# Kernel optimization log

Measured on AMD Instinct MI355X. Metric: run time of the kernel, lower is better.

## Reference

```python
import jax, jax.numpy as jnp
import numpy as np

B, S, D, H, F = 4, 2048, 512, 8, 2048
HD = D // H
EPS = 1e-5


def setup_inputs() -> dict:
    key = jax.random.key(0)
    ks = jax.random.split(key, 12)
    s = lambda fan_in: 1.0 / np.sqrt(fan_in)
    return {
        "x": jax.random.normal(ks[0], (B, S, D), dtype=jnp.float32),
        "Wqkv": jax.random.uniform(ks[1], (D, 3 * D), minval=-s(D), maxval=s(D)),
        "bqkv": jax.random.uniform(ks[2], (3 * D,), minval=-s(D), maxval=s(D)),
        "Wo": jax.random.uniform(ks[3], (D, D), minval=-s(D), maxval=s(D)),
        "bo": jax.random.uniform(ks[4], (D,), minval=-s(D), maxval=s(D)),
        "g1": jnp.ones((D,), jnp.float32),
        "beta1": jnp.zeros((D,), jnp.float32),
        "W1": jax.random.uniform(ks[5], (D, F), minval=-s(D), maxval=s(D)),
        "b1": jax.random.uniform(ks[6], (F,), minval=-s(D), maxval=s(D)),
        "W2": jax.random.uniform(ks[7], (F, D), minval=-s(F), maxval=s(F)),
        "b2": jax.random.uniform(ks[8], (D,), minval=-s(F), maxval=s(F)),
        "g2": jnp.ones((D,), jnp.float32),
        "beta2": jnp.zeros((D,), jnp.float32),
    }


def _layernorm(x, g, b):
    mu = jnp.mean(x, axis=-1, keepdims=True)
    var = jnp.mean(jnp.square(x - mu), axis=-1, keepdims=True)
    return (x - mu) * jax.lax.rsqrt(var + EPS) * g + b


def reference(x, Wqkv, bqkv, Wo, bo, g1, beta1, W1, b1, W2, b2, g2, beta2):
    b, s, d = x.shape
    # QKV projection -> [b, s, 3, H, HD] -> q,k,v each [b, H, s, HD]
    qkv = (x @ Wqkv + bqkv).reshape(b, s, 3, H, HD)
    q, k, v = jnp.moveaxis(qkv, 2, 0)            # [3, b, s, H, HD]
    q = q.transpose(0, 2, 1, 3)
    k = k.transpose(0, 2, 1, 3)
    v = v.transpose(0, 2, 1, 3)
    scores = jnp.einsum('bhqd,bhkd->bhqk', q, k) / np.sqrt(HD).astype(np.float32)
    attn = jax.nn.softmax(scores, axis=-1)
    ctx = jnp.einsum('bhqk,bhkd->bhqd', attn, v)
    ctx = ctx.transpose(0, 2, 1, 3).reshape(b, s, d)
    attn_out = ctx @ Wo + bo
    x = _layernorm(x + attn_out, g1, beta1)
    # FFN (dropout inactive in eval)
    ffn = jax.nn.relu(x @ W1 + b1) @ W2 + b2
    return _layernorm(x + ffn, g2, beta2)
```

## Files before the change

### kernel.cpp

```cpp
#include <hip/hip_runtime.h>
#include <hip/hip_bf16.h>

#define S_ 2048
#define M_ 8192

typedef __bf16 bf16x8 __attribute__((ext_vector_type(8)));
typedef float f32x4 __attribute__((ext_vector_type(4)));

__device__ __forceinline__ void gload16(const void* g, void* l) {
  __builtin_amdgcn_global_load_lds(
      (const __attribute__((address_space(1))) void*)g,
      (__attribute__((address_space(3))) void*)l, 16, 0, 0);
}

template<int CTRL>
__device__ __forceinline__ float dppf(float x) {
  return __int_as_float(__builtin_amdgcn_update_dpp(
      0, __float_as_int(x), CTRL, 0xF, 0xF, true));
}
__device__ __forceinline__ float red16_sum(float x) {
  x += dppf<0x121>(x);
  x += dppf<0x122>(x);
  x += dppf<0x124>(x);
  x += dppf<0x128>(x);
  return x;
}

__global__ __launch_bounds__(256)
void cvt_x_k(const float* __restrict__ x, __bf16* __restrict__ xb) {
  int i = blockIdx.x * 256 + threadIdx.x;
  float4 v = ((const float4*)x)[i];
  union { __bf16 hh[4]; uint2 u; } pk;
  pk.hh[0] = (__bf16)v.x; pk.hh[1] = (__bf16)v.y;
  pk.hh[2] = (__bf16)v.z; pk.hh[3] = (__bf16)v.w;
  ((uint2*)xb)[i] = pk.u;
}

__global__ __launch_bounds__(256)
void tcvt_k(const float* __restrict__ Wm, __bf16* __restrict__ Wt, int K, int N) {
  __shared__ float tile[64][65];
  int nbn = N >> 6;
  int tk = blockIdx.x / nbn, tn = blockIdx.x % nbn;
  int tc = threadIdx.x & 63, tr = threadIdx.x >> 6;
#pragma unroll
  for (int p = 0; p < 16; ++p) {
    int kl = p * 4 + tr;
    tile[kl][tc] = Wm[(size_t)(tk * 64 + kl) * N + tn * 64 + tc];
  }
  __syncthreads();
#pragma unroll
  for (int p = 0; p < 16; ++p) {
    int nl = p * 4 + tr;
    Wt[(size_t)(tn * 64 + nl) * K + tk * 64 + tc] = (__bf16)tile[tc][nl];
  }
}

template<int MODE, int N, int K, int BM, int KS = 1>
__global__ __launch_bounds__(256, 2)
void gemm_k(const __bf16* __restrict__ A, const __bf16* __restrict__ Bt,
            const float* __restrict__ bias,
            float* __restrict__ outf, __bf16* __restrict__ outb,
            __bf16* __restrict__ outq, __bf16* __restrict__ outk,
            __bf16* __restrict__ outv) {
  constexpr int NB = N / 128;
  constexpr int BJ = (BM == 128) ? 4 : 2;
  constexpr int KT = K / KS / 64;
  __shared__ __bf16 As[BM * 64];
  __shared__ __bf16 Bs[128 * 64];

  int id = blockIdx.x;
  int cpx = gridDim.x >> 3;
  int sw = (id & 7) * cpx + (id >> 3);
  int ks = 0;
  if (KS == 2) { ks = sw & 1; sw >>= 1; }
  int mb = sw / NB, nb = sw % NB;

  int t = threadIdx.x;
  int lane = t & 63;
  int g = lane >> 4, c = lane & 15;
  int w = t >> 6;
  int wrow = (BM == 128) ? (w >> 1) * 64 : 0;
  int wcol = (BM == 128) ? (w & 1) * 64 : w * 32;

  const __bf16* Ab = A + (size_t)mb * BM * K + (size_t)ks * (K / KS);
  const __bf16* Bb = Bt + (size_t)nb * 128 * K + (size_t)ks * (K / KS);

  f32x4 acc[4][BJ] = {};

  for (int kt = 0; kt < KT; ++kt) {
#pragma unroll
    for (int it = 0; it < BM / 32; ++it) {
      int idx = it * 256 + t;
      int row = idx >> 3, ch = idx & 7;
      int sch = ch ^ (row & 7);
      gload16(Ab + (size_t)row * K + kt * 64 + sch * 8, (char*)As + idx * 16);
    }
#pragma unroll
    for (int it = 0; it < 4; ++it) {
      int idx = it * 256 + t;
      int row = idx >> 3, ch = idx & 7;
      int sch = ch ^ (row & 7);
      gload16(Bb + (size_t)row * K + kt * 64 + sch * 8, (char*)Bs + idx * 16);
    }
    __syncthreads();
#pragma unroll
    for (int kk = 0; kk < 2; ++kk) {
      bf16x8 af[4], bfv[BJ];
#pragma unroll
      for (int i = 0; i < 4; ++i) {
        int row = wrow + i * 16 + c;
        int ch = (kk * 4 + g) ^ (row & 7);
        af[i] = *(const bf16x8*)((const char*)As + row * 128 + ch * 16);
      }
#pragma unroll
      for (int j = 0; j < BJ; ++j) {
        int row = wcol + j * 16 + c;
        int ch = (kk * 4 + g) ^ (row & 7);
        bfv[j] = *(const bf16x8*)((const char*)Bs + row * 128 + ch * 16);
      }
      __builtin_amdgcn_s_setprio(1);
#pragma unroll
      for (int i = 0; i < 4; ++i)
#pragma unroll
        for (int j = 0; j < BJ; ++j)
          acc[i][j] = __builtin_amdgcn_mfma_f32_16x16x32_bf16(af[i], bfv[j],
                                                              acc[i][j], 0, 0, 0);
      __builtin_amdgcn_s_setprio(0);
    }
    __syncthreads();
  }

  int row0 = mb * BM + wrow;
  int col0 = nb * 128 + wcol;

  if (MODE == 1) {
#pragma unroll
    for (int j = 0; j < BJ; ++j) {
      int col = col0 + j * 16 + c;
      float bv = bias[col];
#pragma unroll
      for (int i = 0; i < 4; ++i)
#pragma unroll
        for (int r = 0; r < 4; ++r) {
          int rr = row0 + i * 16 + g * 4 + r;
          outf[(size_t)rr * N + col] = acc[i][j][r] + bv;
        }
    }
  } else if (MODE == 2 || MODE == 3) {
    __bf16* dst = (KS == 2 && ks == 1) ? outq : outb;
#pragma unroll
    for (int j = 0; j < BJ; ++j) {
      int col = col0 + j * 16 + c;
      float bv = (KS == 2 && ks == 1) ? 0.f : bias[col];
#pragma unroll
      for (int i = 0; i < 4; ++i)
#pragma unroll
        for (int r = 0; r < 4; ++r) {
          int rr = row0 + i * 16 + g * 4 + r;
          float v = acc[i][j][r] + bv;
          if (MODE == 2) v = fmaxf(v, 0.f);
          dst[(size_t)rr * N + col] = (__bf16)v;
        }
    }
  } else {
    int tsel = nb >> 2;
    int h = ((nb & 3) << 1) | (w & 1);
#pragma unroll
    for (int j = 0; j < BJ; ++j) {
      int hd = j * 16 + c;
      float bv = bias[nb * 128 + wcol + j * 16 + c];
#pragma unroll
      for (int i = 0; i < 4; ++i) {
        int rr = row0 + i * 16 + g * 4;
        int b = rr >> 11, s = rr & 2047;
        int bh = b * 8 + h;
        if (tsel == 2) {
          union { __bf16 hh[4]; uint2 u; } pk;
#pragma unroll
          for (int r = 0; r < 4; ++r) pk.hh[r] = (__bf16)(acc[i][j][r] + bv);
          *(uint2*)(outv + ((size_t)bh * 64 + hd) * 2048 + s) = pk.u;
        } else {
          __bf16* dst = (tsel == 0 ? outq : outk);
#pragma unroll
          for (int r = 0; r < 4; ++r)
            dst[((size_t)bh * 2048 + s + r) * 64 + hd] = (__bf16)(acc[i][j][r] + bv);
        }
      }
    }
  }
}

__global__ __launch_bounds__(256, 4)
void attn_k(const __bf16* __restrict__ qb, const __bf16* __restrict__ kb,
            const __bf16* __restrict__ vt, __bf16* __restrict__ ctx) {
  __shared__ __bf16 Ks[2][64 * 64];
  __shared__ __bf16 Vs[2][64 * 64];
  __shared__ char P_lds[4][16 * 128];

  int id = blockIdx.x;
  int sw = (id & 7) * 128 + (id >> 3);
  int bh = sw >> 5, qblk = sw & 31;

  int t = threadIdx.x, lane = t & 63, w = t >> 6;
  int g = lane >> 4, c = lane & 15;

  const __bf16* Q  = qb + (size_t)bh * S_ * 64;
  const __bf16* Kp = kb + (size_t)bh * S_ * 64;
  const __bf16* Vp = vt + (size_t)bh * 64 * S_;

  int q0 = qblk * 64 + w * 16;

  bf16x8 qf[2];
#pragma unroll
  for (int kk = 0; kk < 2; ++kk) {
    bf16x8 v = *(const bf16x8*)(Q + (size_t)(q0 + c) * 64 + kk * 32 + g * 8);
#pragma unroll
    for (int e = 0; e < 8; ++e) v[e] = (__bf16)((float)v[e] * 0.18033688f);
    qf[kk] = v;
  }

  f32x4 o[4] = {};
  float srun[4] = {0.f, 0.f, 0.f, 0.f};

  char* Pw = P_lds[w];
  int kvoff[2];
#pragma unroll
  for (int kk = 0; kk < 2; ++kk)
    kvoff[kk] = c * 128 + ((kk * 4 + g) ^ (c & 7)) * 16;

  auto stage = [&](int kt, int buf) {
    int kbase = kt * 64;
#pragma unroll
    for (int it = 0; it < 2; ++it) {
      int idx = it * 256 + t;
      int row = idx >> 3, ch = idx & 7;
      int sch = ch ^ (row & 7);
      gload16(Kp + (size_t)(kbase + row) * 64 + sch * 8, (char*)Ks[buf] + idx * 16);
      gload16(Vp + (size_t)row * S_ + kbase + sch * 8,   (char*)Vs[buf] + idx * 16);
    }
  };

  stage(0, 0);

  auto step = [&](int kbi, int cur, bool last) {
    if (!last) stage(kbi + 1, cur ^ 1);
    if (last) asm volatile("s_waitcnt vmcnt(0)" ::: "memory");
    else      asm volatile("s_waitcnt vmcnt(4)" ::: "memory");
    __builtin_amdgcn_s_barrier();
    asm volatile("" ::: "memory");
    const char* Kb = (const char*)Ks[cur];
    const char* Vb = (const char*)Vs[cur];

    bf16x8 kf[4][2];
#pragma unroll
    for (int j = 0; j < 4; ++j)
#pragma unroll
      for (int kk = 0; kk < 2; ++kk)
        kf[j][kk] = *(const bf16x8*)(Kb + j * 2048 + kvoff[kk]);
    f32x4 sacc[4] = {};
    __builtin_amdgcn_s_setprio(1);
#pragma unroll
    for (int j = 0; j < 4; ++j) {
      sacc[j] = __builtin_amdgcn_mfma_f32_16x16x32_bf16(qf[0], kf[j][0], sacc[j], 0, 0, 0);
      sacc[j] = __builtin_amdgcn_mfma_f32_16x16x32_bf16(qf[1], kf[j][1], sacc[j], 0, 0, 0);
    }
    __builtin_amdgcn_s_setprio(0);

#pragma unroll
    for (int r = 0; r < 4; ++r) {
      float p0 = exp2f(sacc[0][r]);
      float p1 = exp2f(sacc[1][r]);
      float p2 = exp2f(sacc[2][r]);
      float p3 = exp2f(sacc[3][r]);
      srun[r] += (p0 + p1) + (p2 + p3);
      int prow = g * 4 + r;
      char* base = Pw + prow * 128;
      int sz = (prow & 7) << 4;
      *(__bf16*)(base + ((2 * c) ^ sz))      = (__bf16)p0;
      *(__bf16*)(base + ((32 + 2 * c) ^ sz)) = (__bf16)p1;
      *(__bf16*)(base + ((64 + 2 * c) ^ sz)) = (__bf16)p2;
      *(__bf16*)(base + ((96 + 2 * c) ^ sz)) = (__bf16)p3;
    }
#pragma unroll
    for (int kk = 0; kk < 2; ++kk) {
      int pch = (kk * 4 + g) ^ (c & 7);
      bf16x8 pf = *(const bf16x8*)(Pw + c * 128 + pch * 16);
      __builtin_amdgcn_s_setprio(1);
#pragma unroll
      for (int n = 0; n < 4; ++n) {
        bf16x8 vf = *(const bf16x8*)(Vb + n * 2048 + kvoff[kk]);
        o[n] = __builtin_amdgcn_mfma_f32_16x16x32_bf16(pf, vf, o[n], 0, 0, 0);
      }
      __builtin_amdgcn_s_setprio(0);
    }
    if (!last) {
      asm volatile("" ::: "memory");
      __builtin_amdgcn_s_barrier();
      asm volatile("" ::: "memory");
    }
  };

  for (int kbi = 0; kbi < 30; kbi += 2) {
    step(kbi, 0, false);
    step(kbi + 1, 1, false);
  }
  step(30, 0, false);
  step(31, 1, true);

  int b = bh >> 3, h = bh & 7;
  f32x4 inv;
#pragma unroll
  for (int r = 0; r < 4; ++r) inv[r] = 1.f / red16_sum(srun[r]);
#pragma unroll
  for (int n = 0; n < 4; ++n)
#pragma unroll
    for (int r = 0; r < 4; ++r) {
      int q = q0 + g * 4 + r;
      int d = n * 16 + c;
      ctx[((size_t)(b * 2048 + q)) * 512 + h * 64 + d] = (__bf16)(o[n][r] * inv[r]);
    }
}

template<bool IN1F32, bool WF, bool IN3>
__global__ __launch_bounds__(256)
void ln_k(const float* __restrict__ in1f, const __bf16* __restrict__ in1b,
          const __bf16* __restrict__ in2, const __bf16* __restrict__ in3,
          const float* __restrict__ gam, const float* __restrict__ bet,
          float* __restrict__ outf, __bf16* __restrict__ outb) {
  int w = threadIdx.x >> 6, lane = threadIdx.x & 63;
  int row = blockIdx.x * 4 + w;
  size_t base = (size_t)row * 512 + lane * 8;
  float a[8];
  if (IN1F32) {
    float4 a0 = *(const float4*)(in1f + base);
    float4 a1 = *(const float4*)(in1f + base + 4);
    a[0] = a0.x; a[1] = a0.y; a[2] = a0.z; a[3] = a0.w;
    a[4] = a1.x; a[5] = a1.y; a[6] = a1.z; a[7] = a1.w;
  } else {
    bf16x8 av = *(const bf16x8*)(in1b + base);
#pragma unroll
    for (int k = 0; k < 8; ++k) a[k] = (float)av[k];
  }
  bf16x8 bv = *(const bf16x8*)(in2 + base);
  float x[8];
#pragma unroll
  for (int k = 0; k < 8; ++k) x[k] = a[k] + (float)bv[k];
  if (IN3) {
    bf16x8 cv = *(const bf16x8*)(in3 + base);
#pragma unroll
    for (int k = 0; k < 8; ++k) x[k] += (float)cv[k];
  }
  float s1 = 0.f, s2 = 0.f;
#pragma unroll
  for (int k = 0; k < 8; ++k) { s1 += x[k]; s2 += x[k] * x[k]; }
#pragma unroll
  for (int m = 1; m < 64; m <<= 1) { s1 += __shfl_xor(s1, m); s2 += __shfl_xor(s2, m); }
  float mu = s1 * (1.f / 512.f);
  float var = s2 * (1.f / 512.f) - mu * mu;
  float rs = rsqrtf(var + 1e-5f);
  float4 g0 = *(const float4*)(gam + lane * 8);
  float4 g1 = *(const float4*)(gam + lane * 8 + 4);
  float4 e0 = *(const float4*)(bet + lane * 8);
  float4 e1 = *(const float4*)(bet + lane * 8 + 4);
  float gg[8] = {g0.x, g0.y, g0.z, g0.w, g1.x, g1.y, g1.z, g1.w};
  float bb[8] = {e0.x, e0.y, e0.z, e0.w, e1.x, e1.y, e1.z, e1.w};
  float y[8];
#pragma unroll
  for (int k = 0; k < 8; ++k) y[k] = (x[k] - mu) * rs * gg[k] + bb[k];
  if (WF) {
    float4 o0 = {y[0], y[1], y[2], y[3]};
    float4 o1 = {y[4], y[5], y[6], y[7]};
    *(float4*)(outf + base) = o0;
    *(float4*)(outf + base + 4) = o1;
  } else {
    union { __bf16 hh[8]; uint4 u; } pk;
#pragma unroll
    for (int k = 0; k < 8; ++k) pk.hh[k] = (__bf16)y[k];
    *(uint4*)(outb + base) = pk.u;
  }
}

extern "C" void kernel_launch(void* const* d_in, const int* in_sizes, int n_in,
                              void* d_out, int out_size, void* d_ws, size_t ws_size,
                              hipStream_t stream) {
  (void)in_sizes; (void)n_in; (void)out_size;
  const float* x    = (const float*)d_in[0];
  const float* Wqkv = (const float*)d_in[1];
  const float* bqkv = (const float*)d_in[2];
  const float* Wo   = (const float*)d_in[3];
  const float* bo   = (const float*)d_in[4];
  const float* g1   = (const float*)d_in[5];
  const float* be1  = (const float*)d_in[6];
  const float* W1   = (const float*)d_in[7];
  const float* b1   = (const float*)d_in[8];
  const float* W2   = (const float*)d_in[9];
  const float* b2   = (const float*)d_in[10];
  const float* g2   = (const float*)d_in[11];
  const float* be2  = (const float*)d_in[12];
  float* out = (float*)d_out;

  char* ws = (char*)d_ws;
  size_t off = 0;
  auto alloc = [&](size_t bytes) {
    char* p = ws + off;
    off += (bytes + 255) & ~(size_t)255;
    return p;
  };
  __bf16* xb    = (__bf16*)alloc((size_t)M_ * 512 * 2);
  __bf16* wqkvt = (__bf16*)alloc((size_t)1536 * 512 * 2);
  __bf16* wot   = (__bf16*)alloc((size_t)512 * 512 * 2);
  __bf16* w1t   = (__bf16*)alloc((size_t)2048 * 512 * 2);
  __bf16* w2t   = (__bf16*)alloc((size_t)512 * 2048 * 2);
  __bf16* qbuf  = (__bf16*)alloc((size_t)32 * 2048 * 64 * 2);
  __bf16* kbuf  = (__bf16*)alloc((size_t)32 * 2048 * 64 * 2);
  __bf16* vtbuf = (__bf16*)alloc((size_t)32 * 64 * 2048 * 2);
  __bf16* ctxb  = (__bf16*)alloc((size_t)M_ * 512 * 2);
  __bf16* part0 = (__bf16*)alloc((size_t)M_ * 512 * 2);
  __bf16* part1 = (__bf16*)alloc((size_t)M_ * 512 * 2);
  __bf16* y1b   = (__bf16*)alloc((size_t)M_ * 512 * 2);
  __bf16* h1    = (__bf16*)alloc((size_t)M_ * 2048 * 2);
  if (off > ws_size) return;

  cvt_x_k<<<4096, 256, 0, stream>>>(x, xb);
  tcvt_k<<<192, 256, 0, stream>>>(Wqkv, wqkvt, 512, 1536);
  tcvt_k<<<64, 256, 0, stream>>>(Wo, wot, 512, 512);
  tcvt_k<<<256, 256, 0, stream>>>(W1, w1t, 512, 2048);
  tcvt_k<<<256, 256, 0, stream>>>(W2, w2t, 2048, 512);

  gemm_k<0, 1536, 512, 128><<<768, 256, 0, stream>>>(xb, wqkvt, bqkv, nullptr, nullptr,
                                                     qbuf, kbuf, vtbuf);
  attn_k<<<1024, 256, 0, stream>>>(qbuf, kbuf, vtbuf, ctxb);
  gemm_k<3, 512, 512, 64, 2><<<1024, 256, 0, stream>>>(ctxb, wot, bo, nullptr, part0,
                                                       part1, nullptr, nullptr);
  ln_k<true, false, true><<<2048, 256, 0, stream>>>(x, nullptr, part0, part1, g1, be1,
                                                    nullptr, y1b);
  gemm_k<2, 2048, 512, 128><<<1024, 256, 0, stream>>>(y1b, w1t, b1, nullptr, h1,
                                                      nullptr, nullptr, nullptr);
  gemm_k<3, 512, 2048, 64, 2><<<1024, 256, 0, stream>>>(h1, w2t, b2, nullptr, part0,
                                                        part1, nullptr, nullptr);
  ln_k<false, true, true><<<2048, 256, 0, stream>>>(nullptr, y1b, part0, part1, g2, be2,
                                                    out, nullptr);
}
```

Baseline: 168.6 us.

## Use 32x32 MFMA in attention with register-resident P via permlane swap

Rewrites the attention inner loop to use 32x32x16 MFMAs, computing S^T = K·Q^T so that the probability tile ends up in a register layout usable directly as the A operand of the PV MFMA. The round-trip of P through LDS is replaced by bf16 packing plus v_permlane32_swap. Work is split as a 2x2 grid of waves over query and key halves, so the two key-half partial outputs and row sums are combined through LDS at the end. This removes per-step LDS writes and reads of P and reduces the number of MFMA issues, at the cost of a final cross-wave reduction and more accumulator registers.

```diff
diff --git a/kernel.cpp b/kernel.cpp
--- a/kernel.cpp
+++ b/kernel.cpp
@@ -6,6 +6,8 @@
 
 typedef __bf16 bf16x8 __attribute__((ext_vector_type(8)));
 typedef float f32x4 __attribute__((ext_vector_type(4)));
+typedef float f32x16 __attribute__((ext_vector_type(16)));
+typedef unsigned int u32x4 __attribute__((ext_vector_type(4)));
 
 __device__ __forceinline__ void gload16(const void* g, void* l) {
   __builtin_amdgcn_global_load_lds(
@@ -13,17 +15,10 @@
       (__attribute__((address_space(3))) void*)l, 16, 0, 0);
 }
 
-template<int CTRL>
-__device__ __forceinline__ float dppf(float x) {
-  return __int_as_float(__builtin_amdgcn_update_dpp(
-      0, __float_as_int(x), CTRL, 0xF, 0xF, true));
-}
-__device__ __forceinline__ float red16_sum(float x) {
-  x += dppf<0x121>(x);
-  x += dppf<0x122>(x);
-  x += dppf<0x124>(x);
-  x += dppf<0x128>(x);
-  return x;
+__device__ __forceinline__ unsigned int pkbf(float a, float b) {
+  unsigned short ua = __builtin_bit_cast(unsigned short, (__bf16)a);
+  unsigned short ub = __builtin_bit_cast(unsigned short, (__bf16)b);
+  return (unsigned int)ua | ((unsigned int)ub << 16);
 }
 
 __global__ __launch_bounds__(256)
@@ -195,38 +190,45 @@
             const __bf16* __restrict__ vt, __bf16* __restrict__ ctx) {
   __shared__ __bf16 Ks[2][64 * 64];
   __shared__ __bf16 Vs[2][64 * 64];
-  __shared__ char P_lds[4][16 * 128];
+  __shared__ float srun_l[64];
 
   int id = blockIdx.x;
   int sw = (id & 7) * 128 + (id >> 3);
   int bh = sw >> 5, qblk = sw & 31;
 
   int t = threadIdx.x, lane = t & 63, w = t >> 6;
-  int g = lane >> 4, c = lane & 15;
+  int c32 = lane & 31, h = lane >> 5;
+  int wq = w >> 1, wk = w & 1;
 
   const __bf16* Q  = qb + (size_t)bh * S_ * 64;
   const __bf16* Kp = kb + (size_t)bh * S_ * 64;
   const __bf16* Vp = vt + (size_t)bh * 64 * S_;
 
-  int q0 = qblk * 64 + w * 16;
-
-  bf16x8 qf[2];
-#pragma unroll
-  for (int kk = 0; kk < 2; ++kk) {
-    bf16x8 v = *(const bf16x8*)(Q + (size_t)(q0 + c) * 64 + kk * 32 + g * 8);
+  int q0 = qblk * 64;
+  int qg = q0 + wq * 32 + c32;
+
+  bf16x8 qf[4];
+#pragma unroll
+  for (int c16 = 0; c16 < 4; ++c16) {
+    bf16x8 v = *(const bf16x8*)(Q + (size_t)qg * 64 + c16 * 16 + h * 8);
 #pragma unroll
     for (int e = 0; e < 8; ++e) v[e] = (__bf16)((float)v[e] * 0.18033688f);
-    qf[kk] = v;
-  }
-
-  f32x4 o[4] = {};
-  float srun[4] = {0.f, 0.f, 0.f, 0.f};
-
-  char* Pw = P_lds[w];
-  int kvoff[2];
-#pragma unroll
-  for (int kk = 0; kk < 2; ++kk)
-    kvoff[kk] = c * 128 + ((kk * 4 + g) ^ (c & 7)) * 16;
+    qf[c16] = v;
+  }
+
+  f32x16 o0 = {}, o1 = {};
+  float srun = 0.f;
+
+  int swz = c32 & 7;
+  int krowb = (wk * 32 + c32) * 128;
+  int kchunk[4];
+#pragma unroll
+  for (int c16 = 0; c16 < 4; ++c16)
+    kchunk[c16] = (((c16 * 2 + h)) ^ swz) * 16;
+  int vchunk[2];
+#pragma unroll
+  for (int kc = 0; kc < 2; ++kc)
+    vchunk[kc] = ((wk * 4 + kc * 2 + h) ^ swz) * 16;
 
   auto stage = [&](int kt, int buf) {
     int kbase = kt * 64;
@@ -251,48 +253,43 @@
     const char* Kb = (const char*)Ks[cur];
     const char* Vb = (const char*)Vs[cur];
 
-    bf16x8 kf[4][2];
-#pragma unroll
-    for (int j = 0; j < 4; ++j)
-#pragma unroll
-      for (int kk = 0; kk < 2; ++kk)
-        kf[j][kk] = *(const bf16x8*)(Kb + j * 2048 + kvoff[kk]);
-    f32x4 sacc[4] = {};
+    f32x16 sacc = {};
     __builtin_amdgcn_s_setprio(1);
 #pragma unroll
-    for (int j = 0; j < 4; ++j) {
-      sacc[j] = __builtin_amdgcn_mfma_f32_16x16x32_bf16(qf[0], kf[j][0], sacc[j], 0, 0, 0);
-      sacc[j] = __builtin_amdgcn_mfma_f32_16x16x32_bf16(qf[1], kf[j][1], sacc[j], 0, 0, 0);
+    for (int c16 = 0; c16 < 4; ++c16) {
+      bf16x8 kf = *(const bf16x8*)(Kb + krowb + kchunk[c16]);
+      sacc = __builtin_amdgcn_mfma_f32_32x32x16_bf16(kf, qf[c16], sacc, 0, 0, 0);
     }
     __builtin_amdgcn_s_setprio(0);
 
-#pragma unroll
-    for (int r = 0; r < 4; ++r) {
-      float p0 = exp2f(sacc[0][r]);
-      float p1 = exp2f(sacc[1][r]);
-      float p2 = exp2f(sacc[2][r]);
-      float p3 = exp2f(sacc[3][r]);
-      srun[r] += (p0 + p1) + (p2 + p3);
-      int prow = g * 4 + r;
-      char* base = Pw + prow * 128;
-      int sz = (prow & 7) << 4;
-      *(__bf16*)(base + ((2 * c) ^ sz))      = (__bf16)p0;
-      *(__bf16*)(base + ((32 + 2 * c) ^ sz)) = (__bf16)p1;
-      *(__bf16*)(base + ((64 + 2 * c) ^ sz)) = (__bf16)p2;
-      *(__bf16*)(base + ((96 + 2 * c) ^ sz)) = (__bf16)p3;
-    }
-#pragma unroll
-    for (int kk = 0; kk < 2; ++kk) {
-      int pch = (kk * 4 + g) ^ (c & 7);
-      bf16x8 pf = *(const bf16x8*)(Pw + c * 128 + pch * 16);
-      __builtin_amdgcn_s_setprio(1);
-#pragma unroll
-      for (int n = 0; n < 4; ++n) {
-        bf16x8 vf = *(const bf16x8*)(Vb + n * 2048 + kvoff[kk]);
-        o[n] = __builtin_amdgcn_mfma_f32_16x16x32_bf16(pf, vf, o[n], 0, 0, 0);
-      }
-      __builtin_amdgcn_s_setprio(0);
-    }
+    float p[16];
+#pragma unroll
+    for (int i = 0; i < 16; ++i) { p[i] = exp2f(sacc[i]); srun += p[i]; }
+
+    unsigned int x1 = pkbf(p[0], p[1]),  x2 = pkbf(p[2], p[3]);
+    unsigned int y1 = pkbf(p[4], p[5]),  y2 = pkbf(p[6], p[7]);
+    asm volatile("v_permlane32_swap_b32 %0, %1" : "+v"(y1), "+v"(x1));
+    asm volatile("v_permlane32_swap_b32 %0, %1" : "+v"(y2), "+v"(x2));
+    u32x4 f0 = {x1, x2, y1, y2};
+    bf16x8 pa0 = __builtin_bit_cast(bf16x8, f0);
+    unsigned int x3 = pkbf(p[8], p[9]),   x4 = pkbf(p[10], p[11]);
+    unsigned int y3 = pkbf(p[12], p[13]), y4 = pkbf(p[14], p[15]);
+    asm volatile("v_permlane32_swap_b32 %0, %1" : "+v"(y3), "+v"(x3));
+    asm volatile("v_permlane32_swap_b32 %0, %1" : "+v"(y4), "+v"(x4));
+    u32x4 f1 = {x3, x4, y3, y4};
+    bf16x8 pa1 = __builtin_bit_cast(bf16x8, f1);
+
+    __builtin_amdgcn_s_setprio(1);
+#pragma unroll
+    for (int kc = 0; kc < 2; ++kc) {
+      bf16x8 pa = kc ? pa1 : pa0;
+      bf16x8 va = *(const bf16x8*)(Vb + c32 * 128 + vchunk[kc]);
+      bf16x8 vb = *(const bf16x8*)(Vb + (32 + c32) * 128 + vchunk[kc]);
+      o0 = __builtin_amdgcn_mfma_f32_32x32x16_bf16(pa, va, o0, 0, 0, 0);
+      o1 = __builtin_amdgcn_mfma_f32_32x32x16_bf16(pa, vb, o1, 0, 0, 0);
+    }
+    __builtin_amdgcn_s_setprio(0);
+
     if (!last) {
       asm volatile("" ::: "memory");
       __builtin_amdgcn_s_barrier();
@@ -307,18 +304,34 @@
   step(30, 0, false);
   step(31, 1, true);
 
-  int b = bh >> 3, h = bh & 7;
-  f32x4 inv;
-#pragma unroll
-  for (int r = 0; r < 4; ++r) inv[r] = 1.f / red16_sum(srun[r]);
-#pragma unroll
-  for (int n = 0; n < 4; ++n)
-#pragma unroll
-    for (int r = 0; r < 4; ++r) {
-      int q = q0 + g * 4 + r;
-      int d = n * 16 + c;
-      ctx[((size_t)(b * 2048 + q)) * 512 + h * 64 + d] = (__bf16)(o[n][r] * inv[r]);
-    }
+  srun += __shfl_xor(srun, 32);
+  __syncthreads();
+  float* olds = (float*)Ks;
+  if (wk == 1) {
+#pragma unroll
+    for (int reg = 0; reg < 16; ++reg) {
+      int qrow = (reg & 3) + 8 * (reg >> 2) + 4 * h;
+      olds[wq * 2048 + qrow * 64 + c32]      = o0[reg];
+      olds[wq * 2048 + qrow * 64 + 32 + c32] = o1[reg];
+    }
+    srun_l[wq * 32 + c32] = srun;
+  }
+  __syncthreads();
+  if (wk == 0) {
+    float stot = srun + srun_l[wq * 32 + c32];
+    int b = bh >> 3, hd = bh & 7;
+#pragma unroll
+    for (int reg = 0; reg < 16; ++reg) {
+      int qrow = (reg & 3) + 8 * (reg >> 2) + 4 * h;
+      float inv = 1.f / __shfl(stot, qrow);
+      float s0 = o0[reg] + olds[wq * 2048 + qrow * 64 + c32];
+      float s1 = o1[reg] + olds[wq * 2048 + qrow * 64 + 32 + c32];
+      int qg2 = q0 + wq * 32 + qrow;
+      size_t base = ((size_t)(b * 2048 + qg2)) * 512 + hd * 64;
+      ctx[base + c32]      = (__bf16)(s0 * inv);
+      ctx[base + 32 + c32] = (__bf16)(s1 * inv);
+    }
+  }
 }
 
 template<bool IN1F32, bool WF, bool IN3>
```

After: 166.5 us. Within noise of the previous version (-1.2%).
